# Performance work log

Measured on AMD Instinct MI355X. Metric: run time of the kernel, lower is better.

## Reference

```python
import jax, jax.numpy as jnp
import numpy as np

NUM_HEADS = 12
HEAD_DIM = 64  # d_out // num_heads = 768 // 12


def setup_inputs() -> dict:
    key = jax.random.key(0)
    ks = jax.random.split(key, 6)
    b, s, d = 2, 2048, 768
    x = jax.random.normal(ks[0], (b, s, d), dtype=jnp.float32)
    sc = 1.0 / np.sqrt(d)
    Wq = jax.random.normal(ks[1], (d, d), dtype=jnp.float32) * sc
    Wk = jax.random.normal(ks[2], (d, d), dtype=jnp.float32) * sc
    Wv = jax.random.normal(ks[3], (d, d), dtype=jnp.float32) * sc
    Wo = jax.random.normal(ks[4], (d, d), dtype=jnp.float32) * sc
    bo = jnp.zeros((d,), dtype=jnp.float32)
    return {"x": x, "Wq": Wq, "Wk": Wk, "Wv": Wv, "Wo": Wo, "bo": bo}


def reference(x, Wq, Wk, Wv, Wo, bo):
    # Prefill from a fresh sliding-window KV cache: cache == new K/V,
    # standard causal (triu) mask. dropout=0 (eval).
    b, s, d = x.shape
    H, Dh = NUM_HEADS, HEAD_DIM

    def proj(W):  # torch Linear: x @ W^T, then split heads -> [b, H, s, Dh]
        return (x @ W.T).reshape(b, s, H, Dh).transpose(0, 2, 1, 3)

    q, k, v = proj(Wq), proj(Wk), proj(Wv)

    scores = jnp.einsum('bhqd,bhkd->bhqk', q, k)          # [b,H,s,s]
    causal = jnp.triu(jnp.ones((s, s), dtype=bool), k=1)  # future positions
    scores = jnp.where(causal[None, None], -jnp.inf, scores)
    attn = jax.nn.softmax(scores / np.sqrt(Dh), axis=-1)

    ctx = jnp.einsum('bhqk,bhkd->bhqd', attn, v)          # [b,H,s,Dh]
    ctx = ctx.transpose(0, 2, 1, 3).reshape(b, s, d)      # [b,s,d_out]
    return ctx @ Wo.T + bo
```

## Files before the change

kernel.cpp:

```cpp
#include <hip/hip_runtime.h>
#include <stdint.h>

typedef __attribute__((ext_vector_type(4))) float f32x4;
typedef __attribute__((ext_vector_type(8))) short s16x8;

#if __has_builtin(__builtin_amdgcn_exp2f)
#define EXP2(x) __builtin_amdgcn_exp2f(x)
#else
#define EXP2(x) exp2f(x)
#endif

#define GL2LDS(g, s)                                                        \
  __builtin_amdgcn_global_load_lds(                                         \
      (const __attribute__((address_space(1))) void*)(g),                   \
      (__attribute__((address_space(3))) void*)(s), 16, 0, 0)

__device__ __forceinline__ unsigned short tobf(float x) {
  uint32_t u = __builtin_bit_cast(uint32_t, x);
  u += 0x7fffu + ((u >> 16) & 1u);
  return (unsigned short)(u >> 16);
}

__device__ __forceinline__ uint32_t pk2(float lo, float hi) {
  return (uint32_t)tobf(lo) | ((uint32_t)tobf(hi) << 16);
}

__global__ __launch_bounds__(256) void cvt_all(
    const float* __restrict__ x,  const float* __restrict__ wq,
    const float* __restrict__ wk, const float* __restrict__ wv,
    const float* __restrict__ wo, unsigned short* __restrict__ outb) {
  int i = blockIdx.x * 256 + threadIdx.x;
  if (i >= 1376256) return;
  const float* in;
  int j;
  if (i < 786432) { in = x; j = i; }
  else {
    int k = i - 786432;
    int sel = k / 147456;
    j = k - sel * 147456;
    in = (sel == 0) ? wq : (sel == 1) ? wk : (sel == 2) ? wv : wo;
  }
  float4 v = reinterpret_cast<const float4*>(in)[j];
  uint2 o; o.x = pk2(v.x, v.y); o.y = pk2(v.z, v.w);
  reinterpret_cast<uint2*>(outb)[i] = o;
}

__global__ __launch_bounds__(256) void qkv_gemm(
    const unsigned short* __restrict__ xb,
    const unsigned short* __restrict__ wq,
    const unsigned short* __restrict__ wk,
    const unsigned short* __restrict__ wv,
    unsigned short* __restrict__ q_ws,
    unsigned short* __restrict__ k_ws,
    unsigned short* __restrict__ vt_ws) {
  __shared__ unsigned short As[2][4096];
  __shared__ unsigned short Bs[2][4096];
  const int t = threadIdx.x;
  const int l = t & 63, w = t >> 6;
  const int wm = w >> 1, wn = w & 1;
  const int lr = l & 15, lg = l >> 4;

  const int id = (int)blockIdx.x;
  const int xcd = id & 7;
  const int g = id >> 3;
  const int nt = g % 18;
  const int tileM = ((g / 18) * 8 + xcd) * 128;
  const int wsel = nt / 6;
  const unsigned short* W = (wsel == 0) ? wq : ((wsel == 1) ? wk : wv);
  const int tileN = (nt % 6) * 128;

  const int srow = l >> 2;
  const int scol = ((l & 3) ^ (srow & 3)) * 8;

#define QSTAGE(buf, k0_)                                                       \
  do {                                                                         \
    _Pragma("unroll")                                                          \
    for (int i_ = 0; i_ < 2; ++i_) {                                           \
      GL2LDS(&xb[(tileM + w * 32 + i_ * 16 + srow) * 768 + (k0_) + scol],      \
             &As[buf][w * 1024 + i_ * 512]);                                   \
      GL2LDS(&W [(tileN + w * 32 + i_ * 16 + srow) * 768 + (k0_) + scol],      \
             &Bs[buf][w * 1024 + i_ * 512]);                                   \
    }                                                                          \
  } while (0)

  const int chf = ((lg ^ (lr & 3)) << 3);

  f32x4 acc[4][4];
  const f32x4 z4 = {0.f, 0.f, 0.f, 0.f};
#pragma unroll
  for (int i = 0; i < 4; ++i)
#pragma unroll
    for (int j = 0; j < 4; ++j) acc[i][j] = z4;

  QSTAGE(0, 0);
  __syncthreads();
  int c = 0;
  for (int it = 0; it < 24; ++it) {
    if (it < 23) QSTAGE(c ^ 1, (it + 1) * 32);
    s16x8 a[4], b[4];
#pragma unroll
    for (int mi = 0; mi < 4; ++mi)
      a[mi] = *(const s16x8*)&As[c][(wm * 64 + mi * 16 + lr) * 32 + chf];
#pragma unroll
    for (int ni = 0; ni < 4; ++ni)
      b[ni] = *(const s16x8*)&Bs[c][(wn * 64 + ni * 16 + lr) * 32 + chf];
    __builtin_amdgcn_s_setprio(1);
#pragma unroll
    for (int mi = 0; mi < 4; ++mi)
#pragma unroll
      for (int ni = 0; ni < 4; ++ni)
        acc[mi][ni] = __builtin_amdgcn_mfma_f32_16x16x32_bf16(a[mi], b[ni], acc[mi][ni], 0, 0, 0);
    __builtin_amdgcn_s_setprio(0);
    if (it < 23) {
      __syncthreads();
      c ^= 1;
    }
  }
#undef QSTAGE

#pragma unroll
  for (int mi = 0; mi < 4; ++mi)
#pragma unroll
    for (int ni = 0; ni < 4; ++ni) {
      int m0 = tileM + wm * 64 + mi * 16 + lg * 4;
      int n = tileN + wn * 64 + ni * 16 + lr;
      int bb = m0 >> 11, sq0 = m0 & 2047;
      int h = n >> 6, dh = n & 63;
      if (wsel == 0) {
#pragma unroll
        for (int r = 0; r < 4; ++r)
          q_ws[((bb * 12 + h) * 2048 + sq0 + r) * 64 + dh] =
              tobf(acc[mi][ni][r] * 0.18033688011112042f);
      } else if (wsel == 1) {
#pragma unroll
        for (int r = 0; r < 4; ++r)
          k_ws[((bb * 12 + h) * 2048 + sq0 + r) * 64 + dh] = tobf(acc[mi][ni][r]);
      } else {
        uint2 o;
        o.x = pk2(acc[mi][ni][0], acc[mi][ni][1]);
        o.y = pk2(acc[mi][ni][2], acc[mi][ni][3]);
        *(uint2*)&vt_ws[((bb * 12 + h) * 64 + dh) * 2048 + sq0] = o;
      }
    }
}

__global__ __launch_bounds__(128) void attn_kernel(
    const unsigned short* __restrict__ q_ws,
    const unsigned short* __restrict__ k_ws,
    const unsigned short* __restrict__ vt_ws,
    unsigned short* __restrict__ ctx) {
  __shared__ unsigned short Ks[2][4096];
  __shared__ unsigned short Vs[2][4096];

  const int t = threadIdx.x;
  const int l = t & 63, w = t >> 6;
  const int lr = l & 15, lg = l >> 4;

  const int id = (int)blockIdx.x;
  const int xcd = id & 7;
  const int g = id >> 3;
  const int qt = 63 - g / 3;
  const int bh = (g % 3) * 8 + xcd;

  const int rb = w * 8 + (l >> 3);
  const int gcol = ((l & 7) ^ (l >> 3)) * 8;
  const int krow = 8 * ((rb >> 2) & 3) + (rb & 3);
  const unsigned short* kgp  = &k_ws[(bh * 2048 + krow) * 64 + gcol];
  const unsigned short* vbase = &vt_ws[(bh * 64 + rb) * 2048 + gcol];

#define STAGE(buf, kt_)                                                \
  do {                                                                 \
    GL2LDS(kgp + (kt_) * 4096,           &Ks[buf][w * 512]);           \
    GL2LDS(kgp + (kt_) * 4096 + 2048,    &Ks[buf][1024 + w * 512]);    \
    GL2LDS(kgp + (kt_) * 4096 + 256,     &Ks[buf][2048 + w * 512]);    \
    GL2LDS(kgp + (kt_) * 4096 + 2304,    &Ks[buf][3072 + w * 512]);    \
    GL2LDS(vbase + (kt_) * 64,           &Vs[buf][w * 512]);           \
    GL2LDS(vbase + (kt_) * 64 + 32768,   &Vs[buf][1024 + w * 512]);    \
    GL2LDS(vbase + (kt_) * 64 + 65536,   &Vs[buf][2048 + w * 512]);    \
    GL2LDS(vbase + (kt_) * 64 + 98304,   &Vs[buf][3072 + w * 512]);    \
  } while (0)

  const int cks0 = (lg * 8) ^ ((lr & 7) << 3);
  const int cks1 = (32 + lg * 8) ^ ((lr & 7) << 3);

  const int bb = bh / 12, hh = bh % 12;
  const f32x4 z4 = {0.f, 0.f, 0.f, 0.f};

  const int ktmax = qt >> 1;
  const int qg = qt * 32 + w * 16 + lr;

  s16x8 qa[2];
#pragma unroll
  for (int kk = 0; kk < 2; ++kk)
    qa[kk] = *(const s16x8*)&q_ws[(bh * 2048 + qg) * 64 + kk * 32 + lg * 8];

  f32x4 o[4];
#pragma unroll
  for (int di = 0; di < 4; ++di) o[di] = z4;
  float lrun = 0.f;
  f32x4 s[4];

  STAGE(0, 0);
  __syncthreads();

  __builtin_amdgcn_s_setprio(1);
#pragma unroll
  for (int ni = 0; ni < 4; ++ni) {
    s16x8 kb0 = *(const s16x8*)&Ks[0][ni * 1024 + lr * 64 + cks0];
    s16x8 kb1 = *(const s16x8*)&Ks[0][ni * 1024 + lr * 64 + cks1];
    s[ni] = __builtin_amdgcn_mfma_f32_16x16x32_bf16(kb0, qa[0], z4, 0, 0, 0);
    s[ni] = __builtin_amdgcn_mfma_f32_16x16x32_bf16(kb1, qa[1], s[ni], 0, 0, 0);
  }
  __builtin_amdgcn_s_setprio(0);
  if (ktmax >= 1) STAGE(1, 1);

  int c = 0;
  for (int kt = 0; kt <= ktmax; ++kt) {
    if (kt == ktmax) {
#pragma unroll
      for (int ni = 0; ni < 4; ++ni)
#pragma unroll
        for (int r = 0; r < 4; ++r) {
          int kg_ = kt * 64 + ((ni & 1) << 5) + (lg << 3) + ((ni >> 1) << 2) + r;
          if (kg_ > qg) s[ni][r] = -1e30f;
        }
    }

#pragma unroll
    for (int ni = 0; ni < 4; ++ni)
#pragma unroll
      for (int r = 0; r < 4; ++r) s[ni][r] = EXP2(s[ni][r]);
    {
      float t0 = (s[0][0] + s[0][1]) + (s[0][2] + s[0][3]);
      float t1 = (s[1][0] + s[1][1]) + (s[1][2] + s[1][3]);
      float t2 = (s[2][0] + s[2][1]) + (s[2][2] + s[2][3]);
      float t3 = (s[3][0] + s[3][1]) + (s[3][2] + s[3][3]);
      lrun += (t0 + t1) + (t2 + t3);
    }

    s16x8 pa[2];
#pragma unroll
    for (int kk = 0; kk < 2; ++kk) {
      uint4 u;
      u.x = pk2(s[kk][0],     s[kk][1]);
      u.y = pk2(s[kk][2],     s[kk][3]);
      u.z = pk2(s[kk + 2][0], s[kk + 2][1]);
      u.w = pk2(s[kk + 2][2], s[kk + 2][3]);
      pa[kk] = __builtin_bit_cast(s16x8, u);
    }

    const bool have_next = (kt < ktmax);
    __builtin_amdgcn_s_setprio(1);
    if (have_next) {
      __syncthreads();
#pragma unroll
      for (int ni = 0; ni < 4; ++ni) {
        s16x8 kb0 = *(const s16x8*)&Ks[c ^ 1][ni * 1024 + lr * 64 + cks0];
        s16x8 kb1 = *(const s16x8*)&Ks[c ^ 1][ni * 1024 + lr * 64 + cks1];
        s[ni] = __builtin_amdgcn_mfma_f32_16x16x32_bf16(kb0, qa[0], z4, 0, 0, 0);
        s[ni] = __builtin_amdgcn_mfma_f32_16x16x32_bf16(kb1, qa[1], s[ni], 0, 0, 0);
      }
    }
#pragma unroll
    for (int di = 0; di < 4; ++di) {
      s16x8 vb0 = *(const s16x8*)&Vs[c][di * 1024 + lr * 64 + cks0];
      s16x8 vb1 = *(const s16x8*)&Vs[c][di * 1024 + lr * 64 + cks1];
      o[di] = __builtin_amdgcn_mfma_f32_16x16x32_bf16(vb0, pa[0], o[di], 0, 0, 0);
      o[di] = __builtin_amdgcn_mfma_f32_16x16x32_bf16(vb1, pa[1], o[di], 0, 0, 0);
    }
    __builtin_amdgcn_s_setprio(0);

    if (kt + 2 <= ktmax) {
      __syncthreads();
      STAGE(c, kt + 2);
    }
    c ^= 1;
  }

  float lt = lrun + __shfl_xor(lrun, 16);
  lt += __shfl_xor(lt, 32);
  const float rl = 1.0f / lt;
#pragma unroll
  for (int di = 0; di < 4; ++di) {
    uint2 ov;
    ov.x = pk2(o[di][0] * rl, o[di][1] * rl);
    ov.y = pk2(o[di][2] * rl, o[di][3] * rl);
    *(uint2*)&ctx[(bb * 2048 + qg) * 768 + hh * 64 + di * 16 + lg * 4] = ov;
  }
#undef STAGE
}

__global__ __launch_bounds__(256) void out_gemm(
    const unsigned short* __restrict__ ctxb,
    const unsigned short* __restrict__ wo,
    const float* __restrict__ bo,
    float* __restrict__ out) {
  __shared__ unsigned short As[2][4096];
  __shared__ unsigned short Bs[2][4096];
  const int t = threadIdx.x;
  const int l = t & 63, w = t >> 6;
  const int wm = w >> 1, wn = w & 1;
  const int lr = l & 15, lg = l >> 4;

  const int id = (int)blockIdx.x;
  const int xcd = id & 7;
  const int g = id >> 3;
  const int tileM = ((g / 6) * 8 + xcd) * 128;
  const int tileN = (g % 6) * 128;

  const int srow = l >> 2;
  const int scol = ((l & 3) ^ (srow & 3)) * 8;

#define OSTAGE(buf, k0_)                                                       \
  do {                                                                         \
    _Pragma("unroll")                                                          \
    for (int i_ = 0; i_ < 2; ++i_) {                                           \
      GL2LDS(&ctxb[(tileM + w * 32 + i_ * 16 + srow) * 768 + (k0_) + scol],    \
             &As[buf][w * 1024 + i_ * 512]);                                   \
      GL2LDS(&wo  [(tileN + w * 32 + i_ * 16 + srow) * 768 + (k0_) + scol],    \
             &Bs[buf][w * 1024 + i_ * 512]);                                   \
    }                                                                          \
  } while (0)

  const int chf = ((lg ^ (lr & 3)) << 3);

  f32x4 acc[4][4];
  const f32x4 z4 = {0.f, 0.f, 0.f, 0.f};
#pragma unroll
  for (int i = 0; i < 4; ++i)
#pragma unroll
    for (int j = 0; j < 4; ++j) acc[i][j] = z4;

  OSTAGE(0, 0);
  __syncthreads();
  int c = 0;
  for (int it = 0; it < 24; ++it) {
    if (it < 23) OSTAGE(c ^ 1, (it + 1) * 32);
    s16x8 a[4], b[4];
#pragma unroll
    for (int mi = 0; mi < 4; ++mi)
      a[mi] = *(const s16x8*)&As[c][(wm * 64 + mi * 16 + lr) * 32 + chf];
#pragma unroll
    for (int ni = 0; ni < 4; ++ni)
      b[ni] = *(const s16x8*)&Bs[c][(wn * 64 + ni * 16 + lr) * 32 + chf];
    __builtin_amdgcn_s_setprio(1);
#pragma unroll
    for (int mi = 0; mi < 4; ++mi)
#pragma unroll
      for (int ni = 0; ni < 4; ++ni)
        acc[mi][ni] = __builtin_amdgcn_mfma_f32_16x16x32_bf16(a[mi], b[ni], acc[mi][ni], 0, 0, 0);
    __builtin_amdgcn_s_setprio(0);
    if (it < 23) {
      __syncthreads();
      c ^= 1;
    }
  }
#undef OSTAGE

#pragma unroll
  for (int mi = 0; mi < 4; ++mi)
#pragma unroll
    for (int ni = 0; ni < 4; ++ni)
#pragma unroll
      for (int r = 0; r < 4; ++r) {
        int m = tileM + wm * 64 + mi * 16 + lg * 4 + r;
        int n = tileN + wn * 64 + ni * 16 + lr;
        out[m * 768 + n] = acc[mi][ni][r] + bo[n];
      }
}

extern "C" void kernel_launch(void* const* d_in, const int* in_sizes, int n_in,
                              void* d_out, int out_size, void* d_ws, size_t ws_size,
                              hipStream_t stream) {
  const float* x  = (const float*)d_in[0];
  const float* Wq = (const float*)d_in[1];
  const float* Wk = (const float*)d_in[2];
  const float* Wv = (const float*)d_in[3];
  const float* Wo = (const float*)d_in[4];
  const float* bo = (const float*)d_in[5];
  float* out = (float*)d_out;

  char* ws = (char*)d_ws;
  unsigned short* xb    = (unsigned short*)(ws);
  unsigned short* wqb   = (unsigned short*)(ws + 6291456);
  unsigned short* wkb   = (unsigned short*)(ws + 7471104);
  unsigned short* wvb   = (unsigned short*)(ws + 8650752);
  unsigned short* wob   = (unsigned short*)(ws + 9830400);
  unsigned short* q_ws  = (unsigned short*)(ws + 11010048);
  unsigned short* k_ws  = (unsigned short*)(ws + 17301504);
  unsigned short* vt_ws = (unsigned short*)(ws + 23592960);
  unsigned short* ctx   = (unsigned short*)(ws + 29884416);

  cvt_all<<<5376, 256, 0, stream>>>(x, Wq, Wk, Wv, Wo, (unsigned short*)ws);
  qkv_gemm<<<576, 256, 0, stream>>>(xb, wqb, wkb, wvb, q_ws, k_ws, vt_ws);
  attn_kernel<<<1536, 128, 0, stream>>>(q_ws, k_ws, vt_ws, ctx);
  out_gemm<<<192, 256, 0, stream>>>(ctx, wob, bo, out);
}
```

Baseline: 88.52 us.

## Halve attention KV tile to 32 keys and pack P by truncation

Cuts the attention kernel's K/V tile from 64 to 32 keys per iteration, which halves LDS use and rewrites the staging index maps and MFMA operand layout to match. The loop runs twice as many iterations, so causal masking now wastes less work on the last diagonal tile. Probabilities are packed to bf16 with a single byte-permute truncation instead of round-to-nearest. In exchange there are more barriers and loop iterations per block, and truncation adds a slight accuracy bias.

```diff
diff --git a/kernel.cpp b/kernel.cpp
--- a/kernel.cpp
+++ b/kernel.cpp
@@ -23,6 +23,11 @@
 
 __device__ __forceinline__ uint32_t pk2(float lo, float hi) {
   return (uint32_t)tobf(lo) | ((uint32_t)tobf(hi) << 16);
+}
+
+__device__ __forceinline__ uint32_t pktrunc(float lo, float hi) {
+  return __builtin_amdgcn_perm(__builtin_bit_cast(uint32_t, hi),
+                               __builtin_bit_cast(uint32_t, lo), 0x07060302u);
 }
 
 __global__ __launch_bounds__(256) void cvt_all(
@@ -149,8 +154,8 @@
     const unsigned short* __restrict__ k_ws,
     const unsigned short* __restrict__ vt_ws,
     unsigned short* __restrict__ ctx) {
-  __shared__ unsigned short Ks[2][4096];
-  __shared__ unsigned short Vs[2][4096];
+  __shared__ unsigned short Ks[2][2048];
+  __shared__ unsigned short Vs[2][2048];
 
   const int t = threadIdx.x;
   const int l = t & 63, w = t >> 6;
@@ -162,22 +167,23 @@
   const int qt = 63 - g / 3;
   const int bh = (g % 3) * 8 + xcd;
 
-  const int rb = w * 8 + (l >> 3);
-  const int gcol = ((l & 7) ^ (l >> 3)) * 8;
-  const int krow = 8 * ((rb >> 2) & 3) + (rb & 3);
-  const unsigned short* kgp  = &k_ws[(bh * 2048 + krow) * 64 + gcol];
-  const unsigned short* vbase = &vt_ws[(bh * 64 + rb) * 2048 + gcol];
-
-#define STAGE(buf, kt_)                                                \
-  do {                                                                 \
-    GL2LDS(kgp + (kt_) * 4096,           &Ks[buf][w * 512]);           \
-    GL2LDS(kgp + (kt_) * 4096 + 2048,    &Ks[buf][1024 + w * 512]);    \
-    GL2LDS(kgp + (kt_) * 4096 + 256,     &Ks[buf][2048 + w * 512]);    \
-    GL2LDS(kgp + (kt_) * 4096 + 2304,    &Ks[buf][3072 + w * 512]);    \
-    GL2LDS(vbase + (kt_) * 64,           &Vs[buf][w * 512]);           \
-    GL2LDS(vbase + (kt_) * 64 + 32768,   &Vs[buf][1024 + w * 512]);    \
-    GL2LDS(vbase + (kt_) * 64 + 65536,   &Vs[buf][2048 + w * 512]);    \
-    GL2LDS(vbase + (kt_) * 64 + 98304,   &Vs[buf][3072 + w * 512]);    \
+  const int rl8 = l >> 3;
+  const int p0 = w * 8 + rl8;
+  const int gch = (l & 7) ^ rl8;
+  const int tk0 = (((p0 >> 2) & 3) << 3) + (((p0 >> 4) & 1) << 2) + (p0 & 3);
+  const unsigned short* kb0p = &k_ws[(bh * 2048 + tk0) * 64 + gch * 8];
+  const unsigned short* kb1p = &k_ws[(bh * 2048 + tk0 + 4) * 64 + gch * 8];
+  const int vd0 = p0 + 32 * (gch >> 2);
+  const int vkc = (gch & 3) * 8;
+  const unsigned short* vb0p = &vt_ws[(bh * 64 + vd0) * 2048 + vkc];
+  const unsigned short* vb1p = &vt_ws[(bh * 64 + vd0 + 16) * 2048 + vkc];
+
+#define STAGE(buf, kt_)                                          \
+  do {                                                           \
+    GL2LDS(kb0p + (kt_) * 2048, &Ks[buf][w * 512]);              \
+    GL2LDS(kb1p + (kt_) * 2048, &Ks[buf][1024 + w * 512]);       \
+    GL2LDS(vb0p + (kt_) * 32,   &Vs[buf][w * 512]);              \
+    GL2LDS(vb1p + (kt_) * 32,   &Vs[buf][1024 + w * 512]);       \
   } while (0)
 
   const int cks0 = (lg * 8) ^ ((lr & 7) << 3);
@@ -186,7 +192,7 @@
   const int bb = bh / 12, hh = bh % 12;
   const f32x4 z4 = {0.f, 0.f, 0.f, 0.f};
 
-  const int ktmax = qt >> 1;
+  const int ktmax = qt;
   const int qg = qt * 32 + w * 16 + lr;
 
   s16x8 qa[2];
@@ -198,18 +204,18 @@
 #pragma unroll
   for (int di = 0; di < 4; ++di) o[di] = z4;
   float lrun = 0.f;
-  f32x4 s[4];
+  f32x4 s[2];
 
   STAGE(0, 0);
   __syncthreads();
 
   __builtin_amdgcn_s_setprio(1);
 #pragma unroll
-  for (int ni = 0; ni < 4; ++ni) {
-    s16x8 kb0 = *(const s16x8*)&Ks[0][ni * 1024 + lr * 64 + cks0];
-    s16x8 kb1 = *(const s16x8*)&Ks[0][ni * 1024 + lr * 64 + cks1];
-    s[ni] = __builtin_amdgcn_mfma_f32_16x16x32_bf16(kb0, qa[0], z4, 0, 0, 0);
-    s[ni] = __builtin_amdgcn_mfma_f32_16x16x32_bf16(kb1, qa[1], s[ni], 0, 0, 0);
+  for (int ni = 0; ni < 2; ++ni) {
+    s16x8 ka = *(const s16x8*)&Ks[0][(ni * 16 + lr) * 64 + cks0];
+    s16x8 kb = *(const s16x8*)&Ks[0][(ni * 16 + lr) * 64 + cks1];
+    s[ni] = __builtin_amdgcn_mfma_f32_16x16x32_bf16(ka, qa[0], z4, 0, 0, 0);
+    s[ni] = __builtin_amdgcn_mfma_f32_16x16x32_bf16(kb, qa[1], s[ni], 0, 0, 0);
   }
   __builtin_amdgcn_s_setprio(0);
   if (ktmax >= 1) STAGE(1, 1);
@@ -218,55 +224,44 @@
   for (int kt = 0; kt <= ktmax; ++kt) {
     if (kt == ktmax) {
 #pragma unroll
-      for (int ni = 0; ni < 4; ++ni)
+      for (int ni = 0; ni < 2; ++ni)
 #pragma unroll
         for (int r = 0; r < 4; ++r) {
-          int kg_ = kt * 64 + ((ni & 1) << 5) + (lg << 3) + ((ni >> 1) << 2) + r;
+          int kg_ = kt * 32 + (lg << 3) + (ni << 2) + r;
           if (kg_ > qg) s[ni][r] = -1e30f;
         }
     }
 
 #pragma unroll
-    for (int ni = 0; ni < 4; ++ni)
+    for (int ni = 0; ni < 2; ++ni)
 #pragma unroll
       for (int r = 0; r < 4; ++r) s[ni][r] = EXP2(s[ni][r]);
-    {
-      float t0 = (s[0][0] + s[0][1]) + (s[0][2] + s[0][3]);
-      float t1 = (s[1][0] + s[1][1]) + (s[1][2] + s[1][3]);
-      float t2 = (s[2][0] + s[2][1]) + (s[2][2] + s[2][3]);
-      float t3 = (s[3][0] + s[3][1]) + (s[3][2] + s[3][3]);
-      lrun += (t0 + t1) + (t2 + t3);
-    }
-
-    s16x8 pa[2];
-#pragma unroll
-    for (int kk = 0; kk < 2; ++kk) {
-      uint4 u;
-      u.x = pk2(s[kk][0],     s[kk][1]);
-      u.y = pk2(s[kk][2],     s[kk][3]);
-      u.z = pk2(s[kk + 2][0], s[kk + 2][1]);
-      u.w = pk2(s[kk + 2][2], s[kk + 2][3]);
-      pa[kk] = __builtin_bit_cast(s16x8, u);
-    }
+    lrun += ((s[0][0] + s[0][1]) + (s[0][2] + s[0][3])) +
+            ((s[1][0] + s[1][1]) + (s[1][2] + s[1][3]));
+
+    uint4 u;
+    u.x = pktrunc(s[0][0], s[0][1]);
+    u.y = pktrunc(s[0][2], s[0][3]);
+    u.z = pktrunc(s[1][0], s[1][1]);
+    u.w = pktrunc(s[1][2], s[1][3]);
+    s16x8 pa = __builtin_bit_cast(s16x8, u);
 
     const bool have_next = (kt < ktmax);
     __builtin_amdgcn_s_setprio(1);
     if (have_next) {
       __syncthreads();
 #pragma unroll
-      for (int ni = 0; ni < 4; ++ni) {
-        s16x8 kb0 = *(const s16x8*)&Ks[c ^ 1][ni * 1024 + lr * 64 + cks0];
-        s16x8 kb1 = *(const s16x8*)&Ks[c ^ 1][ni * 1024 + lr * 64 + cks1];
-        s[ni] = __builtin_amdgcn_mfma_f32_16x16x32_bf16(kb0, qa[0], z4, 0, 0, 0);
-        s[ni] = __builtin_amdgcn_mfma_f32_16x16x32_bf16(kb1, qa[1], s[ni], 0, 0, 0);
+      for (int ni = 0; ni < 2; ++ni) {
+        s16x8 ka = *(const s16x8*)&Ks[c ^ 1][(ni * 16 + lr) * 64 + cks0];
+        s16x8 kb = *(const s16x8*)&Ks[c ^ 1][(ni * 16 + lr) * 64 + cks1];
+        s[ni] = __builtin_amdgcn_mfma_f32_16x16x32_bf16(ka, qa[0], z4, 0, 0, 0);
+        s[ni] = __builtin_amdgcn_mfma_f32_16x16x32_bf16(kb, qa[1], s[ni], 0, 0, 0);
       }
     }
 #pragma unroll
     for (int di = 0; di < 4; ++di) {
-      s16x8 vb0 = *(const s16x8*)&Vs[c][di * 1024 + lr * 64 + cks0];
-      s16x8 vb1 = *(const s16x8*)&Vs[c][di * 1024 + lr * 64 + cks1];
-      o[di] = __builtin_amdgcn_mfma_f32_16x16x32_bf16(vb0, pa[0], o[di], 0, 0, 0);
-      o[di] = __builtin_amdgcn_mfma_f32_16x16x32_bf16(vb1, pa[1], o[di], 0, 0, 0);
+      s16x8 vb = *(const s16x8*)&Vs[c][((di & 1) * 16 + lr) * 64 + (di < 2 ? cks0 : cks1)];
+      o[di] = __builtin_amdgcn_mfma_f32_16x16x32_bf16(vb, pa, o[di], 0, 0, 0);
     }
     __builtin_amdgcn_s_setprio(0);
 
```

After: 96.47 us. 9.0% more time.
